# Performance work log

Hardware: AMD Instinct MI355X
Metric: run time of the kernel (lower is better)

The kernel has to match this reference:

```python
import jax, jax.numpy as jnp
import numpy as np

D = 2048
N_HID = 512
ATT = 512
BATCH = 256
L = 196


def setup_inputs() -> dict:
    key = jax.random.key(0)
    ks = jax.random.split(key, 8)
    s = 0.02
    return {
        "feature": jax.random.normal(ks[0], (BATCH, L, D), dtype=jnp.float32),
        "prev_h": jax.random.normal(ks[1], (BATCH, N_HID), dtype=jnp.float32),
        "W_enc": jax.random.normal(ks[2], (D, ATT), dtype=jnp.float32) * s,
        "b_enc": jnp.zeros((ATT,), dtype=jnp.float32),
        "W_dec": jax.random.normal(ks[3], (N_HID, ATT), dtype=jnp.float32) * s,
        "b_dec": jnp.zeros((ATT,), dtype=jnp.float32),
        "W_tot": jax.random.normal(ks[4], (ATT, 1), dtype=jnp.float32) * s,
        "b_tot": jnp.zeros((1,), dtype=jnp.float32),
    }


def reference(feature, prev_h, W_enc, b_enc, W_dec, b_dec, W_tot, b_tot):
    # att1: (N, L, A); att2: (N, A)
    att1 = jnp.einsum("nld,da->nla", feature, W_enc) + b_enc
    att2 = prev_h @ W_dec + b_dec
    att = jax.nn.relu(att1 + att2[:, None, :])          # (N, L, A)
    scores = (att @ W_tot)[..., 0] + b_tot[0]           # (N, L)
    alpha = jax.nn.softmax(scores, axis=1)              # (N, L)
    weighted_feature = jnp.einsum("nld,nl->nd", feature, alpha)  # (N, D)
    return weighted_feature, alpha
```

## Files before the change

### kernel.cpp

```cpp
#include <hip/hip_runtime.h>
#include <hip/hip_bf16.h>


typedef unsigned short u16;
typedef __attribute__((ext_vector_type(8))) short short8;
typedef __attribute__((ext_vector_type(4))) float f32x4;

#define BATCH 256
#define LQ    196
#define DDIM  2048
#define ADIM  512
#define MTOT  (BATCH * LQ)
#define WF_N  (BATCH * DDIM)
#define KQP   1032

__device__ __forceinline__ u16 f2bf(float f) {
  unsigned u = __builtin_bit_cast(unsigned, f);
  return (u16)((u + 0x7FFFu + ((u >> 16) & 1u)) >> 16);
}

__device__ __forceinline__ ushort4 cvt4(float4 f) {
  ushort4 r;
  r.x = f2bf(f.x); r.y = f2bf(f.y); r.z = f2bf(f.z); r.w = f2bf(f.w);
  return r;
}

__device__ __forceinline__ void glds16(const u16* g, u16* l) {
  __builtin_amdgcn_global_load_lds(
      (const __attribute__((address_space(1))) unsigned int*)g,
      (__attribute__((address_space(3))) unsigned int*)l, 16, 0, 0);
}

__global__ void prepB_k(const float* __restrict__ W_enc, u16* __restrict__ Bst) {
  const int ks = blockIdx.x;
  const int tid = threadIdx.x;
  __shared__ u16 ldsT[32 * 520];
  for (int i4 = tid; i4 < 4096; i4 += 256) {
    int dl = i4 >> 7;
    int nn = (i4 & 127) << 2;
    float4 f = *(const float4*)(W_enc + (size_t)(ks * 32 + dl) * 512 + nn);
    *(ushort4*)(&ldsT[dl * 520 + nn]) = cvt4(f);
  }
  __syncthreads();
  for (int idx = tid; idx < 16384; idx += 256) {
    int kq = idx >> 12;
    int n  = (idx >> 3) & 511;
    int e  = idx & 7;
    Bst[(size_t)ks * 16384 + idx] = ldsT[(kq * 8 + e) * 520 + n];
  }
}

__global__ void att2_k(const float* __restrict__ prev_h,
                       const float* __restrict__ W_dec,
                       const float* __restrict__ b_dec,
                       const float* __restrict__ b_enc,
                       float* __restrict__ att2) {
  const int n = blockIdx.x, tid = threadIdx.x;
  __shared__ float ph[512];
  ph[tid]       = prev_h[n * 512 + tid];
  ph[tid + 256] = prev_h[n * 512 + tid + 256];
  __syncthreads();
  float a0 = b_dec[tid] + b_enc[tid];
  float a1 = b_dec[tid + 256] + b_enc[tid + 256];
  #pragma unroll 8
  for (int h = 0; h < 512; h++) {
    float p = ph[h];
    a0 = fmaf(p, W_dec[h * 512 + tid], a0);
    a1 = fmaf(p, W_dec[h * 512 + tid + 256], a1);
  }
  att2[n * 512 + tid] = a0;
  att2[n * 512 + tid + 256] = a1;
}

__global__ void zero_scores_k(float* __restrict__ s) {
  s[blockIdx.x * 256 + threadIdx.x] = 0.f;
}

__global__ __launch_bounds__(256, 3) void score_gemm_k(
    const float* __restrict__ feature, const u16* __restrict__ Bst,
    const float* __restrict__ att2, const float* __restrict__ W_tot,
    float* __restrict__ scores) {
  __shared__ __align__(16) u16 sA[2][4 * KQP];
  __shared__ __align__(16) u16 sB[2][4 * KQP];
  __shared__ float sRed[2][128];

  const int tid = threadIdx.x;
  const int b = blockIdx.x;
  const int mt = (b >> 5) * 8 + (b & 7);
  const int nt = (b >> 3) & 3;
  const int r0 = mt << 7, n0 = nt << 7;
  const int wid = tid >> 6, lane = tid & 63;
  const int wgm = wid >> 1, wgn = wid & 1;
  const int quad = lane >> 4, cid = lane & 15;

  const int arow = tid >> 3, akk4 = tid & 7;
  const float* gA = feature + (size_t)(r0 + arow) * 2048 + akk4 * 4;
  const int wAoff = (akk4 >> 1) * KQP + (arow << 3) + ((akk4 & 1) << 2);

  const u16* gBlane = Bst + (size_t)wid * 4096 + ((size_t)n0 << 3) + lane * 8;

  const int abase = quad * KQP + (((wgm << 6) + cid) << 3);
  const int bbase = quad * KQP + (((wgn << 6) + cid) << 3);

  f32x4 zero = {0.f, 0.f, 0.f, 0.f};
  f32x4 acc[4][4];
  #pragma unroll
  for (int i = 0; i < 4; i++)
    #pragma unroll
    for (int j = 0; j < 4; j++) acc[i][j] = zero;

  float4 a0, a1, a2, a3;
  {
    const float* p = gA;
    a0 = *(const float4*)(p);
    a1 = *(const float4*)(p + 32 * 2048);
    a2 = *(const float4*)(p + 64 * 2048);
    a3 = *(const float4*)(p + 96 * 2048);
    u16* dst = &sB[0][wid * KQP];
    glds16(gBlane, dst);
    glds16(gBlane + 512, dst + 512);
  }

  for (int ks = 0; ks < 64; ks++) {
    const int buf = ks & 1;
    u16* wa = &sA[buf][wAoff];
    *(ushort4*)(wa)       = cvt4(a0);
    *(ushort4*)(wa + 256) = cvt4(a1);
    *(ushort4*)(wa + 512) = cvt4(a2);
    *(ushort4*)(wa + 768) = cvt4(a3);
    __syncthreads();

    if (ks < 63) {
      const float* p = gA + (ks + 1) * 32;
      a0 = *(const float4*)(p);
      a1 = *(const float4*)(p + 32 * 2048);
      a2 = *(const float4*)(p + 64 * 2048);
      a3 = *(const float4*)(p + 96 * 2048);
      const u16* src = gBlane + (size_t)(ks + 1) * 16384;
      u16* dst = &sB[buf ^ 1][wid * KQP];
      glds16(src, dst);
      glds16(src + 512, dst + 512);
    }

    const u16* sa = &sA[buf][abase];
    const u16* sb = &sB[buf][bbase];
    short8 af[4], bfr[4];
    #pragma unroll
    for (int mi = 0; mi < 4; mi++)
      af[mi] = *(const short8*)(sa + (mi << 7));
    #pragma unroll
    for (int ni = 0; ni < 4; ni++)
      bfr[ni] = *(const short8*)(sb + (ni << 7));
    #pragma unroll
    for (int mi = 0; mi < 4; mi++)
      #pragma unroll
      for (int ni = 0; ni < 4; ni++)
        acc[mi][ni] = __builtin_amdgcn_mfma_f32_16x16x32_bf16(
            af[mi], bfr[ni], acc[mi][ni], 0, 0, 0);
  }

  float wt[4];
  #pragma unroll
  for (int ni = 0; ni < 4; ni++)
    wt[ni] = W_tot[n0 + (wgn << 6) + ni * 16 + cid];

  #pragma unroll
  for (int mi = 0; mi < 4; mi++) {
    #pragma unroll
    for (int reg = 0; reg < 4; reg++) {
      int row_local = (wgm << 6) + mi * 16 + quad * 4 + reg;
      int row_flat = r0 + row_local;
      int nb = row_flat / 196;
      const float* a2r = att2 + nb * 512 + n0 + (wgn << 6);
      float s = 0.f;
      #pragma unroll
      for (int ni = 0; ni < 4; ni++) {
        float v = acc[mi][ni][reg] + a2r[ni * 16 + cid];
        s += fmaxf(v, 0.f) * wt[ni];
      }
      s += __shfl_xor(s, 1); s += __shfl_xor(s, 2);
      s += __shfl_xor(s, 4); s += __shfl_xor(s, 8);
      if (cid == 0) sRed[wgn][row_local] = s;
    }
  }
  __syncthreads();
  if (tid < 128) atomicAdd(&scores[r0 + tid], sRed[0][tid] + sRed[1][tid]);
}

__global__ void softmax_k(const float* __restrict__ scores,
                          float* __restrict__ alpha) {
  const int n = blockIdx.x, tid = threadIdx.x;
  __shared__ float red[8];
  float s = (tid < LQ) ? scores[n * LQ + tid] : -1e30f;
  float m = s;
  for (int o = 32; o; o >>= 1) m = fmaxf(m, __shfl_xor(m, o));
  if ((tid & 63) == 0) red[tid >> 6] = m;
  __syncthreads();
  m = fmaxf(fmaxf(red[0], red[1]), fmaxf(red[2], red[3]));
  float e = (tid < LQ) ? __expf(s - m) : 0.f;
  float t = e;
  for (int o = 32; o; o >>= 1) t += __shfl_xor(t, o);
  if ((tid & 63) == 0) red[4 + (tid >> 6)] = t;
  __syncthreads();
  t = red[4] + red[5] + red[6] + red[7];
  if (tid < LQ) alpha[n * LQ + tid] = e / t;
}

__global__ void wsum_k(const float* __restrict__ feature,
                       const float* __restrict__ alpha,
                       float* __restrict__ out) {
  const int n = blockIdx.x >> 1, half = blockIdx.x & 1;
  const int tid = threadIdx.x;
  __shared__ float al[LQ];
  if (tid < LQ) al[tid] = alpha[n * LQ + tid];
  __syncthreads();
  const float* fp = feature + (size_t)n * LQ * DDIM + half * 1024 + tid * 4;
  float4 acc = {0.f, 0.f, 0.f, 0.f};
  #pragma unroll 4
  for (int l = 0; l < LQ; l++) {
    float a = al[l];
    float4 f = *(const float4*)(fp + (size_t)l * DDIM);
    acc.x = fmaf(a, f.x, acc.x); acc.y = fmaf(a, f.y, acc.y);
    acc.z = fmaf(a, f.z, acc.z); acc.w = fmaf(a, f.w, acc.w);
  }
  *(float4*)(out + n * DDIM + half * 1024 + tid * 4) = acc;
}

extern "C" void kernel_launch(void* const* d_in, const int* in_sizes, int n_in,
                              void* d_out, int out_size, void* d_ws, size_t ws_size,
                              hipStream_t stream) {
  const float* feature = (const float*)d_in[0];
  const float* prev_h  = (const float*)d_in[1];
  const float* W_enc   = (const float*)d_in[2];
  const float* b_enc   = (const float*)d_in[3];
  const float* W_dec   = (const float*)d_in[4];
  const float* b_dec   = (const float*)d_in[5];
  const float* W_tot   = (const float*)d_in[6];

  float* out   = (float*)d_out;
  float* wf    = out;
  float* alpha = out + WF_N;

  char* ws = (char*)d_ws;
  u16*   Bst    = (u16*)ws;
  float* att2   = (float*)(ws + (2u << 20));
  float* scores = (float*)(ws + (2u << 20) + (512u << 10));

  prepB_k<<<64, 256, 0, stream>>>(W_enc, Bst);
  att2_k<<<256, 256, 0, stream>>>(prev_h, W_dec, b_dec, b_enc, att2);
  zero_scores_k<<<196, 256, 0, stream>>>(scores);
  score_gemm_k<<<1568, 256, 0, stream>>>(feature, Bst, att2, W_tot, scores);
  softmax_k<<<256, 256, 0, stream>>>(scores, alpha);
  wsum_k<<<512, 256, 0, stream>>>(feature, alpha, wf);
}
```

Measured before the change: 775.9 us.

## Pre-convert feature to bf16 once and reuse it in GEMM and weighted sum

```diff
diff --git a/kernel.cpp b/kernel.cpp
--- a/kernel.cpp
+++ b/kernel.cpp
@@ -4,6 +4,7 @@
 
 typedef unsigned short u16;
 typedef __attribute__((ext_vector_type(8))) short short8;
+typedef __attribute__((ext_vector_type(8))) unsigned short u16x8;
 typedef __attribute__((ext_vector_type(4))) float f32x4;
 
 #define BATCH 256
@@ -18,35 +19,51 @@
   unsigned u = __builtin_bit_cast(unsigned, f);
   return (u16)((u + 0x7FFFu + ((u >> 16) & 1u)) >> 16);
 }
-
+__device__ __forceinline__ float bf2f(u16 x) {
+  return __builtin_bit_cast(float, (unsigned)x << 16);
+}
 __device__ __forceinline__ ushort4 cvt4(float4 f) {
   ushort4 r;
   r.x = f2bf(f.x); r.y = f2bf(f.y); r.z = f2bf(f.z); r.w = f2bf(f.w);
   return r;
 }
-
 __device__ __forceinline__ void glds16(const u16* g, u16* l) {
   __builtin_amdgcn_global_load_lds(
       (const __attribute__((address_space(1))) unsigned int*)g,
       (__attribute__((address_space(3))) unsigned int*)l, 16, 0, 0);
 }
 
-__global__ void prepB_k(const float* __restrict__ W_enc, u16* __restrict__ Bst) {
-  const int ks = blockIdx.x;
-  const int tid = threadIdx.x;
-  __shared__ u16 ldsT[32 * 520];
-  for (int i4 = tid; i4 < 4096; i4 += 256) {
-    int dl = i4 >> 7;
-    int nn = (i4 & 127) << 2;
-    float4 f = *(const float4*)(W_enc + (size_t)(ks * 32 + dl) * 512 + nn);
-    *(ushort4*)(&ldsT[dl * 520 + nn]) = cvt4(f);
-  }
-  __syncthreads();
-  for (int idx = tid; idx < 16384; idx += 256) {
-    int kq = idx >> 12;
-    int n  = (idx >> 3) & 511;
-    int e  = idx & 7;
-    Bst[(size_t)ks * 16384 + idx] = ldsT[(kq * 8 + e) * 520 + n];
+__global__ void cvtA_k(const float* __restrict__ f, u16* __restrict__ o) {
+  size_t i = (size_t)blockIdx.x * 256 + threadIdx.x;
+  const size_t stride = (size_t)12544 * 256;
+  #pragma unroll
+  for (int k = 0; k < 4; k++, i += stride) {
+    const float4* p = (const float4*)(f + i * 8);
+    float4 x = p[0], y = p[1];
+    ushort4 a = cvt4(x), b = cvt4(y);
+    u16x8 v = {a.x, a.y, a.z, a.w, b.x, b.y, b.z, b.w};
+    *(u16x8*)(o + i * 8) = v;
+  }
+}
+
+__global__ void prepBT_k(const float* __restrict__ W_enc, u16* __restrict__ WencT) {
+  const int dt = blockIdx.x >> 3;
+  const int at = blockIdx.x & 7;
+  const int tid = threadIdx.x;
+  __shared__ u16 t[64][72];
+  const int r = tid >> 2, c4 = tid & 3;
+  #pragma unroll
+  for (int k = 0; k < 4; k++) {
+    int c = (c4 + k * 4) * 4;
+    float4 v = *(const float4*)(W_enc + (size_t)(dt * 64 + r) * 512 + at * 64 + c);
+    *(ushort4*)&t[r][c] = cvt4(v);
+  }
+  __syncthreads();
+  #pragma unroll
+  for (int k = 0; k < 4; k++) {
+    int d = c4 * 16 + k * 4;
+    ushort4 v = {t[d][r], t[d + 1][r], t[d + 2][r], t[d + 3][r]};
+    *(ushort4*)(WencT + (size_t)(at * 64 + r) * 2048 + dt * 64 + d) = v;
   }
 }
 
@@ -76,12 +93,12 @@
   s[blockIdx.x * 256 + threadIdx.x] = 0.f;
 }
 
-__global__ __launch_bounds__(256, 3) void score_gemm_k(
-    const float* __restrict__ feature, const u16* __restrict__ Bst,
+__global__ __launch_bounds__(256, 4) void score_gemm_k(
+    const u16* __restrict__ featB, const u16* __restrict__ WencT,
     const float* __restrict__ att2, const float* __restrict__ W_tot,
     float* __restrict__ scores) {
-  __shared__ __align__(16) u16 sA[2][4 * KQP];
-  __shared__ __align__(16) u16 sB[2][4 * KQP];
+  __shared__ __align__(16) u16 sA[2][4096];
+  __shared__ __align__(16) u16 sB[2][4096];
   __shared__ float sRed[2][128];
 
   const int tid = threadIdx.x;
@@ -93,14 +110,11 @@
   const int wgm = wid >> 1, wgn = wid & 1;
   const int quad = lane >> 4, cid = lane & 15;
 
-  const int arow = tid >> 3, akk4 = tid & 7;
-  const float* gA = feature + (size_t)(r0 + arow) * 2048 + akk4 * 4;
-  const int wAoff = (akk4 >> 1) * KQP + (arow << 3) + ((akk4 & 1) << 2);
-
-  const u16* gBlane = Bst + (size_t)wid * 4096 + ((size_t)n0 << 3) + lane * 8;
-
-  const int abase = quad * KQP + (((wgm << 6) + cid) << 3);
-  const int bbase = quad * KQP + (((wgn << 6) + cid) << 3);
+  const u16* gA0 = featB + (size_t)(r0 + lane) * 2048 + wid * 8;
+  const u16* gB0 = WencT + (size_t)(n0 + lane) * 2048 + wid * 8;
+
+  const int abase = (quad << 10) + (((wgm << 6) + cid) << 3);
+  const int bbase = (quad << 10) + (((wgn << 6) + cid) << 3);
 
   f32x4 zero = {0.f, 0.f, 0.f, 0.f};
   f32x4 acc[4][4];
@@ -109,39 +123,28 @@
     #pragma unroll
     for (int j = 0; j < 4; j++) acc[i][j] = zero;
 
-  float4 a0, a1, a2, a3;
   {
-    const float* p = gA;
-    a0 = *(const float4*)(p);
-    a1 = *(const float4*)(p + 32 * 2048);
-    a2 = *(const float4*)(p + 64 * 2048);
-    a3 = *(const float4*)(p + 96 * 2048);
-    u16* dst = &sB[0][wid * KQP];
-    glds16(gBlane, dst);
-    glds16(gBlane + 512, dst + 512);
-  }
-
+    u16* dA = &sA[0][wid << 10];
+    u16* dB = &sB[0][wid << 10];
+    glds16(gA0, dA);
+    glds16(gA0 + 64 * 2048, dA + 512);
+    glds16(gB0, dB);
+    glds16(gB0 + 64 * 2048, dB + 512);
+  }
+
+  #pragma unroll 2
   for (int ks = 0; ks < 64; ks++) {
     const int buf = ks & 1;
-    u16* wa = &sA[buf][wAoff];
-    *(ushort4*)(wa)       = cvt4(a0);
-    *(ushort4*)(wa + 256) = cvt4(a1);
-    *(ushort4*)(wa + 512) = cvt4(a2);
-    *(ushort4*)(wa + 768) = cvt4(a3);
     __syncthreads();
-
     if (ks < 63) {
-      const float* p = gA + (ks + 1) * 32;
-      a0 = *(const float4*)(p);
-      a1 = *(const float4*)(p + 32 * 2048);
-      a2 = *(const float4*)(p + 64 * 2048);
-      a3 = *(const float4*)(p + 96 * 2048);
-      const u16* src = gBlane + (size_t)(ks + 1) * 16384;
-      u16* dst = &sB[buf ^ 1][wid * KQP];
-      glds16(src, dst);
-      glds16(src + 512, dst + 512);
+      const int o = (ks + 1) << 5;
+      u16* dA = &sA[buf ^ 1][wid << 10];
+      u16* dB = &sB[buf ^ 1][wid << 10];
+      glds16(gA0 + o, dA);
+      glds16(gA0 + o + 64 * 2048, dA + 512);
+      glds16(gB0 + o, dB);
+      glds16(gB0 + o + 64 * 2048, dB + 512);
     }
-
     const u16* sa = &sA[buf][abase];
     const u16* sb = &sB[buf][bbase];
     short8 af[4], bfr[4];
@@ -206,9 +209,151 @@
   if (tid < LQ) alpha[n * LQ + tid] = e / t;
 }
 
-__global__ void wsum_k(const float* __restrict__ feature,
-                       const float* __restrict__ alpha,
-                       float* __restrict__ out) {
+__global__ void wsum_bf16_k(const u16* __restrict__ featB,
+                            const float* __restrict__ alpha,
+                            float* __restrict__ out) {
+  const int n = blockIdx.x >> 1, half = blockIdx.x & 1;
+  const int tid = threadIdx.x;
+  __shared__ float al[LQ];
+  if (tid < LQ) al[tid] = alpha[n * LQ + tid];
+  __syncthreads();
+  const u16* fp = featB + (size_t)n * LQ * DDIM + half * 1024 + tid * 4;
+  float ax = 0.f, ay = 0.f, az = 0.f, aw = 0.f;
+  #pragma unroll 4
+  for (int l = 0; l < LQ; l++) {
+    float a = al[l];
+    ushort4 u = *(const ushort4*)(fp + (size_t)l * DDIM);
+    ax = fmaf(a, bf2f(u.x), ax);
+    ay = fmaf(a, bf2f(u.y), ay);
+    az = fmaf(a, bf2f(u.z), az);
+    aw = fmaf(a, bf2f(u.w), aw);
+  }
+  float4 r = {ax, ay, az, aw};
+  *(float4*)(out + n * DDIM + half * 1024 + tid * 4) = r;
+}
+
+__global__ void prepB_slow_k(const float* __restrict__ W_enc, u16* __restrict__ Bst) {
+  const int ks = blockIdx.x;
+  const int tid = threadIdx.x;
+  __shared__ u16 ldsT[32 * 520];
+  for (int i4 = tid; i4 < 4096; i4 += 256) {
+    int dl = i4 >> 7;
+    int nn = (i4 & 127) << 2;
+    float4 f = *(const float4*)(W_enc + (size_t)(ks * 32 + dl) * 512 + nn);
+    *(ushort4*)(&ldsT[dl * 520 + nn]) = cvt4(f);
+  }
+  __syncthreads();
+  for (int idx = tid; idx < 16384; idx += 256) {
+    int kq = idx >> 12;
+    int n  = (idx >> 3) & 511;
+    int e  = idx & 7;
+    Bst[(size_t)ks * 16384 + idx] = ldsT[(kq * 8 + e) * 520 + n];
+  }
+}
+
+__global__ __launch_bounds__(256, 3) void score_gemm_slow_k(
+    const float* __restrict__ feature, const u16* __restrict__ Bst,
+    const float* __restrict__ att2, const float* __restrict__ W_tot,
+    float* __restrict__ scores) {
+  __shared__ __align__(16) u16 sA[2][4 * KQP];
+  __shared__ __align__(16) u16 sB[2][4 * KQP];
+  __shared__ float sRed[2][128];
+  const int tid = threadIdx.x;
+  const int b = blockIdx.x;
+  const int mt = (b >> 5) * 8 + (b & 7);
+  const int nt = (b >> 3) & 3;
+  const int r0 = mt << 7, n0 = nt << 7;
+  const int wid = tid >> 6, lane = tid & 63;
+  const int wgm = wid >> 1, wgn = wid & 1;
+  const int quad = lane >> 4, cid = lane & 15;
+  const int arow = tid >> 3, akk4 = tid & 7;
+  const float* gA = feature + (size_t)(r0 + arow) * 2048 + akk4 * 4;
+  const int wAoff = (akk4 >> 1) * KQP + (arow << 3) + ((akk4 & 1) << 2);
+  const u16* gBlane = Bst + (size_t)wid * 4096 + ((size_t)n0 << 3) + lane * 8;
+  const int abase = quad * KQP + (((wgm << 6) + cid) << 3);
+  const int bbase = quad * KQP + (((wgn << 6) + cid) << 3);
+  f32x4 zero = {0.f, 0.f, 0.f, 0.f};
+  f32x4 acc[4][4];
+  #pragma unroll
+  for (int i = 0; i < 4; i++)
+    #pragma unroll
+    for (int j = 0; j < 4; j++) acc[i][j] = zero;
+  float4 a0, a1, a2, a3;
+  {
+    const float* p = gA;
+    a0 = *(const float4*)(p);
+    a1 = *(const float4*)(p + 32 * 2048);
+    a2 = *(const float4*)(p + 64 * 2048);
+    a3 = *(const float4*)(p + 96 * 2048);
+    u16* dst = &sB[0][wid * KQP];
+    glds16(gBlane, dst);
+    glds16(gBlane + 512, dst + 512);
+  }
+  for (int ks = 0; ks < 64; ks++) {
+    const int buf = ks & 1;
+    u16* wa = &sA[buf][wAoff];
+    *(ushort4*)(wa)       = cvt4(a0);
+    *(ushort4*)(wa + 256) = cvt4(a1);
+    *(ushort4*)(wa + 512) = cvt4(a2);
+    *(ushort4*)(wa + 768) = cvt4(a3);
+    __syncthreads();
+    if (ks < 63) {
+      const float* p = gA + (ks + 1) * 32;
+      a0 = *(const float4*)(p);
+      a1 = *(const float4*)(p + 32 * 2048);
+      a2 = *(const float4*)(p + 64 * 2048);
+      a3 = *(const float4*)(p + 96 * 2048);
+      const u16* src = gBlane + (size_t)(ks + 1) * 16384;
+      u16* dst = &sB[buf ^ 1][wid * KQP];
+      glds16(src, dst);
+      glds16(src + 512, dst + 512);
+    }
+    const u16* sa = &sA[buf][abase];
+    const u16* sb = &sB[buf][bbase];
+    short8 af[4], bfr[4];
+    #pragma unroll
+    for (int mi = 0; mi < 4; mi++)
+      af[mi] = *(const short8*)(sa + (mi << 7));
+    #pragma unroll
+    for (int ni = 0; ni < 4; ni++)
+      bfr[ni] = *(const short8*)(sb + (ni << 7));
+    #pragma unroll
+    for (int mi = 0; mi < 4; mi++)
+      #pragma unroll
+      for (int ni = 0; ni < 4; ni++)
+        acc[mi][ni] = __builtin_amdgcn_mfma_f32_16x16x32_bf16(
+            af[mi], bfr[ni], acc[mi][ni], 0, 0, 0);
+  }
+  float wt[4];
+  #pragma unroll
+  for (int ni = 0; ni < 4; ni++)
+    wt[ni] = W_tot[n0 + (wgn << 6) + ni * 16 + cid];
+  #pragma unroll
+  for (int mi = 0; mi < 4; mi++) {
+    #pragma unroll
+    for (int reg = 0; reg < 4; reg++) {
+      int row_local = (wgm << 6) + mi * 16 + quad * 4 + reg;
+      int row_flat = r0 + row_local;
+      int nb = row_flat / 196;
+      const float* a2r = att2 + nb * 512 + n0 + (wgn << 6);
+      float s = 0.f;
+      #pragma unroll
+      for (int ni = 0; ni < 4; ni++) {
+        float v = acc[mi][ni][reg] + a2r[ni * 16 + cid];
+        s += fmaxf(v, 0.f) * wt[ni];
+      }
+      s += __shfl_xor(s, 1); s += __shfl_xor(s, 2);
+      s += __shfl_xor(s, 4); s += __shfl_xor(s, 8);
+      if (cid == 0) sRed[wgn][row_local] = s;
+    }
+  }
+  __syncthreads();
+  if (tid < 128) atomicAdd(&scores[r0 + tid], sRed[0][tid] + sRed[1][tid]);
+}
+
+__global__ void wsum_f32_k(const float* __restrict__ feature,
+                           const float* __restrict__ alpha,
+                           float* __restrict__ out) {
   const int n = blockIdx.x >> 1, half = blockIdx.x & 1;
   const int tid = threadIdx.x;
   __shared__ float al[LQ];
@@ -242,14 +387,32 @@
   float* alpha = out + WF_N;
 
   char* ws = (char*)d_ws;
-  u16*   Bst    = (u16*)ws;
-  float* att2   = (float*)(ws + (2u << 20));
-  float* scores = (float*)(ws + (2u << 20) + (512u << 10));
-
-  prepB_k<<<64, 256, 0, stream>>>(W_enc, Bst);
-  att2_k<<<256, 256, 0, stream>>>(prev_h, W_dec, b_dec, b_enc, att2);
-  zero_scores_k<<<196, 256, 0, stream>>>(scores);
-  score_gemm_k<<<1568, 256, 0, stream>>>(feature, Bst, att2, W_tot, scores);
-  softmax_k<<<256, 256, 0, stream>>>(scores, alpha);
-  wsum_k<<<512, 256, 0, stream>>>(feature, alpha, wf);
-}
+  const size_t featB_bytes = (size_t)MTOT * DDIM * 2;
+  const size_t need = featB_bytes + (2u << 20) + (512u << 10) + (256u << 10);
+
+  if (ws_size >= need) {
+    u16*   featB  = (u16*)ws;
+    u16*   WencT  = (u16*)(ws + featB_bytes);
+    float* att2   = (float*)(ws + featB_bytes + (2u << 20));
+    float* scores = (float*)(ws + featB_bytes + (2u << 20) + (512u << 10));
+
+    cvtA_k<<<12544, 256, 0, stream>>>(feature, featB);
+    prepBT_k<<<256, 256, 0, stream>>>(W_enc, WencT);
+    att2_k<<<256, 256, 0, stream>>>(prev_h, W_dec, b_dec, b_enc, att2);
+    zero_scores_k<<<196, 256, 0, stream>>>(scores);
+    score_gemm_k<<<1568, 256, 0, stream>>>(featB, WencT, att2, W_tot, scores);
+    softmax_k<<<256, 256, 0, stream>>>(scores, alpha);
+    wsum_bf16_k<<<512, 256, 0, stream>>>(featB, alpha, wf);
+  } else {
+    u16*   Bst    = (u16*)ws;
+    float* att2   = (float*)(ws + (2u << 20));
+    float* scores = (float*)(ws + (2u << 20) + (512u << 10));
+
+    prepB_slow_k<<<64, 256, 0, stream>>>(W_enc, Bst);
+    att2_k<<<256, 256, 0, stream>>>(prev_h, W_dec, b_dec, b_enc, att2);
+    zero_scores_k<<<196, 256, 0, stream>>>(scores);
+    score_gemm_slow_k<<<1568, 256, 0, stream>>>(feature, Bst, att2, W_tot, scores);
+    softmax_k<<<256, 256, 0, stream>>>(scores, alpha);
+    wsum_f32_k<<<512, 256, 0, stream>>>(feature, alpha, wf);
+  }
+}
```

New measurement: 861.6 us. +11.0%, slower.
